# Kernel tuning notes

Measured on AMD Instinct MI355X. Metric: run time of the kernel, lower is better.

Reference implementation:

```python
import jax, jax.numpy as jnp
import numpy as np

B, S, E, H, D, P = 4, 2048, 1024, 16, 64, 64  # batch, seq, embed, heads, head_dim, position_dim
MASKED_BIAS = -10000.0


def setup_inputs() -> dict:
    key = jax.random.key(0)
    ks = jax.random.split(key, 24)
    n = lambda k, sh: jax.random.normal(k, sh, dtype=jnp.float32)
    eyeD = jnp.eye(D, dtype=jnp.float32)
    eyeH = jnp.eye(H, dtype=jnp.float32)
    inp = {
        'hidden_states': n(ks[0], (B, S, E)),
        'position_states': n(ks[1], (B, S, P)),
        # Conv2D per-head projections (identity init + perturbation): [H, D, D]
        'Wq': eyeD[None] + 0.02 * n(ks[2], (H, D, D)), 'bq': 0.01 * n(ks[3], (H, D)),
        'Wk': eyeD[None] + 0.02 * n(ks[4], (H, D, D)), 'bk': 0.01 * n(ks[5], (H, D)),
        'Wv': eyeD[None] + 0.02 * n(ks[6], (H, D, D)), 'bv': 0.01 * n(ks[7], (H, D)),
        # Conv2D(transpose=True) cross-head mix: weight [H_out, H_in, D], bias [H, D]
        'Wqh': eyeH[:, :, None] + 0.02 * n(ks[8], (H, H, D)), 'bqh': 0.01 * n(ks[9], (H, D)),
        'Wkh': eyeH[:, :, None] + 0.02 * n(ks[10], (H, H, D)), 'bkh': 0.01 * n(ks[11], (H, D)),
        'Wvh': eyeH[:, :, None] + 0.02 * n(ks[12], (H, H, D)), 'bvh': 0.01 * n(ks[13], (H, D)),
        # p_attn Conv1D: position_dim -> 3*head_dim
        'Wp': 0.02 * n(ks[14], (P, 3 * D)), 'bp': 0.01 * n(ks[15], (3 * D,)),
        # position_conv expand: weight [3, 1, H], bias [H]
        'Wpe': 0.02 * n(ks[16], (3, 1, H)), 'bpe': 0.01 * n(ks[17], (H,)),
        # c_proj Conv1D: E -> E
        'Wc': 0.02 * n(ks[18], (E, E)), 'bc': 0.01 * n(ks[19], (E,)),
    }
    return inp


def _attention(hidden_states, position_states, Wq, bq, Wqh, bqh, Wk, bk, Wkh, bkh,
               Wv, bv, Wvh, bvh, Wp, bp, Wpe, bpe, Wc, bc):
    b, s, _ = hidden_states.shape
    x = hidden_states.reshape(b, s, H, D)

    def proj(Wa, ba, Wh, bh):
        # Conv2D: per-head linear within head_dim
        y = jnp.einsum('bshd,hde->bshe', x, Wa) + ba
        # Conv2D(transpose): mix across heads, per feature dim d
        return jnp.einsum('bshd,ghd->bsgd', y, Wh) + bh

    q = proj(Wq, bq, Wqh, bqh)  # [b,s,H,D]
    k = proj(Wk, bk, Wkh, bkh)
    v = proj(Wv, bv, Wvh, bvh)

    # p_attn (Conv1D) -> [b,s,3,D]; p_expand broadcasts each var across heads
    p = (position_states @ Wp + bp).reshape(b, s, 3, D)
    pe = p[..., None, :] * Wpe[:, 0, :][:, :, None] + bpe[:, None]  # [b,s,3,H,D]
    q = q + pe[:, :, 0]
    k = k + pe[:, :, 1]
    v = v + pe[:, :, 2]

    q = q.transpose(0, 2, 1, 3)  # [b,H,s,D]
    k = k.transpose(0, 2, 1, 3)
    v = v.transpose(0, 2, 1, 3)

    scores = jnp.einsum('bhqd,bhkd->bhqk', q, k) / jnp.sqrt(jnp.float32(D))
    causal = jnp.tril(jnp.ones((s, s), dtype=bool))
    scores = jnp.where(causal, scores, jnp.float32(MASKED_BIAS))
    w = jax.nn.softmax(scores, axis=-1)
    o = jnp.einsum('bhqk,bhkd->bhqd', w, v)
    o = o.transpose(0, 2, 1, 3).reshape(b, s, E)
    return o @ Wc + bc


def reference(hidden_states, position_states, Wq, bq, Wqh, bqh, Wk, bk, Wkh, bkh,
              Wv, bv, Wvh, bvh, Wp, bp, Wpe, bpe, Wc, bc):
    return _attention(hidden_states, position_states, Wq, bq, Wqh, bqh, Wk, bk,
                      Wkh, bkh, Wv, bv, Wvh, bvh, Wp, bp, Wpe, bpe, Wc, bc)
```

## Files before the change

kernel.cpp:

```cpp
#include <hip/hip_runtime.h>
#include <stdint.h>
#include <stddef.h>

using bf16x8 = __attribute__((ext_vector_type(8))) __bf16;
using f32x4  = __attribute__((ext_vector_type(4))) float;
using u16x8  = __attribute__((ext_vector_type(8))) unsigned short;
using u16x4  = __attribute__((ext_vector_type(4))) unsigned short;
typedef unsigned short u16;

#define DEV __device__ __forceinline__

#define QSCALE 0.18033688011112042f
#define SBIAS 32.0f

DEV u16 f2bf(float f) {
  unsigned u = __float_as_uint(f);
  u += 0x7fffu + ((u >> 16) & 1u);
  return (u16)(u >> 16);
}

DEV void gld_lds16(const u16* g, u16* l) {
  __builtin_amdgcn_global_load_lds(
      (__attribute__((address_space(1))) void*)g,
      (__attribute__((address_space(3))) void*)l, 16, 0, 0);
}

__global__ __launch_bounds__(256) void k_packA(const float* __restrict__ hs,
                                               const float* __restrict__ ps,
                                               u16* __restrict__ A) {
  int idx = blockIdx.x * 256 + threadIdx.x;
  int t  = idx / 272;
  int c4 = (idx - t * 272) * 4;
  float4 f;
  if (c4 < 1024) f = *(const float4*)(hs + (size_t)t * 1024 + c4);
  else           f = *(const float4*)(ps + (size_t)t * 64 + (c4 - 1024));
  u16x4 o4;
  o4[0] = f2bf(f.x); o4[1] = f2bf(f.y); o4[2] = f2bf(f.z); o4[3] = f2bf(f.w);
  *(u16x4*)(A + (size_t)t * 1088 + c4) = o4;
}

__global__ __launch_bounds__(256) void k_buildW(const float* __restrict__ Wq, const float* __restrict__ Wk,
                                                const float* __restrict__ Wv, const float* __restrict__ Wqh,
                                                const float* __restrict__ Wkh, const float* __restrict__ Wvh,
                                                const float* __restrict__ Wp, const float* __restrict__ Wpe,
                                                u16* __restrict__ Wt) {
  int idx = blockIdx.x * 256 + threadIdx.x;
  int n = idx / 1088, kk = idx - n * 1088;
  int which = n >> 10, g = (n >> 6) & 15, e = n & 63;
  const float* Wa = (which == 0) ? Wq : (which == 1) ? Wk : Wv;
  const float* Wh = (which == 0) ? Wqh : (which == 1) ? Wkh : Wvh;
  float val;
  if (kk < 1024) {
    int h = kk >> 6, d = kk & 63;
    val = Wa[(size_t)(h * 64 + d) * 64 + e] * Wh[(size_t)(g * 16 + h) * 64 + e];
  } else {
    int p = kk - 1024;
    val = Wp[(size_t)p * 192 + which * 64 + e] * Wpe[which * 16 + g];
  }
  if (which == 0) val *= QSCALE;
  Wt[idx] = f2bf(val);
}

__global__ __launch_bounds__(256) void k_buildBias(const float* __restrict__ bq, const float* __restrict__ bk,
                                                   const float* __restrict__ bv, const float* __restrict__ Wqh,
                                                   const float* __restrict__ Wkh, const float* __restrict__ Wvh,
                                                   const float* __restrict__ bqh, const float* __restrict__ bkh,
                                                   const float* __restrict__ bvh, const float* __restrict__ bp,
                                                   const float* __restrict__ Wpe, const float* __restrict__ bpe,
                                                   float* __restrict__ bias) {
  int n = blockIdx.x * 256 + threadIdx.x;
  int which = n >> 10, g = (n >> 6) & 15, e = n & 63;
  const float* ba = (which == 0) ? bq : (which == 1) ? bk : bv;
  const float* Wh = (which == 0) ? Wqh : (which == 1) ? Wkh : Wvh;
  const float* bh = (which == 0) ? bqh : (which == 1) ? bkh : bvh;
  float s = bh[g * 64 + e] + bp[which * 64 + e] * Wpe[which * 16 + g] + bpe[g];
  for (int h = 0; h < 16; ++h) s += ba[h * 64 + e] * Wh[(g * 16 + h) * 64 + e];
  if (which == 0) s *= QSCALE;
  bias[n] = s;
}

__global__ __launch_bounds__(256) void k_transWc(const float* __restrict__ Wc, u16* __restrict__ WcT) {
  __shared__ float tile[32][33];
  int tx = threadIdx.x & 31, ty = threadIdx.x >> 5;
  int n0 = blockIdx.x * 32, k0 = blockIdx.y * 32;
#pragma unroll
  for (int i = 0; i < 32; i += 8)
    tile[ty + i][tx] = Wc[(size_t)(k0 + ty + i) * 1024 + n0 + tx];
  __syncthreads();
#pragma unroll
  for (int i = 0; i < 32; i += 8)
    WcT[(size_t)(n0 + ty + i) * 1024 + k0 + tx] = f2bf(tile[tx][ty + i]);
}

template <int EPI>
__global__ __launch_bounds__(256) void gemm128(const u16* __restrict__ A, const u16* __restrict__ Bt,
                                               const float* __restrict__ bias,
                                               u16* __restrict__ qo, u16* __restrict__ ko, u16* __restrict__ vo,
                                               float* __restrict__ outf, int M, int N, int K) {
  __shared__ alignas(16) u16 As[128 * 64];
  __shared__ alignas(16) u16 Bs[128 * 64];
  const int tid = threadIdx.x;
  const int l = tid & 63, w = tid >> 6;
  const int lr = l & 15, lg = l >> 4;
  const int wm = w >> 1, wn = w & 1;
  const int m0 = blockIdx.y * 128, n0 = blockIdx.x * 128;

  f32x4 acc[4][4] = {};
  const int KT = K >> 6;
  for (int kt = 0; kt < KT; ++kt) {
#pragma unroll
    for (int call = 0; call < 4; ++call) {
      int ci = (call * 4 + w) * 64 + l;
      int row = ci >> 3, s = ci & 7;
      int kq = (s ^ (row & 7)) * 8;
      gld_lds16(A + (size_t)(m0 + row) * K + kt * 64 + kq, &As[(call * 4 + w) * 512]);
      gld_lds16(Bt + (size_t)(n0 + row) * K + kt * 64 + kq, &Bs[(call * 4 + w) * 512]);
    }
    __syncthreads();
#pragma unroll
    for (int kk = 0; kk < 2; ++kk) {
      bf16x8 af[4], bfr[4];
#pragma unroll
      for (int mf = 0; mf < 4; ++mf) {
        int row = wm * 64 + mf * 16 + lr;
        int byo = row * 128 + (((kk * 32 + lg * 8) * 2) ^ ((row & 7) << 4));
        af[mf] = *(const bf16x8*)((const char*)As + byo);
      }
#pragma unroll
      for (int nf = 0; nf < 4; ++nf) {
        int row = wn * 64 + nf * 16 + lr;
        int byo = row * 128 + (((kk * 32 + lg * 8) * 2) ^ ((row & 7) << 4));
        bfr[nf] = *(const bf16x8*)((const char*)Bs + byo);
      }
#pragma unroll
      for (int mf = 0; mf < 4; ++mf)
#pragma unroll
        for (int nf = 0; nf < 4; ++nf)
          acc[mf][nf] = __builtin_amdgcn_mfma_f32_16x16x32_bf16(af[mf], bfr[nf], acc[mf][nf], 0, 0, 0);
    }
    __syncthreads();
  }
#pragma unroll
  for (int mf = 0; mf < 4; ++mf)
#pragma unroll
    for (int nf = 0; nf < 4; ++nf)
#pragma unroll
      for (int r = 0; r < 4; ++r) {
        int row = m0 + wm * 64 + mf * 16 + lg * 4 + r;
        int col = n0 + wn * 64 + nf * 16 + lr;
        float val = acc[mf][nf][r] + bias[col];
        if (EPI == 0) {
          int which = col >> 10, g = (col >> 6) & 15, e = col & 63;
          int b = row >> 11, si = row & 2047;
          size_t idx = ((size_t)((b * 16 + g) * 2048 + si)) * 64 + e;
          u16 bvv = f2bf(val);
          if (which == 0) qo[idx] = bvv;
          else if (which == 1) ko[idx] = bvv;
          else vo[idx] = bvv;
        } else {
          outf[(size_t)row * N + col] = val;
        }
      }
}

__global__ __launch_bounds__(256) void k_transV(const u16* __restrict__ v, u16* __restrict__ vT) {
  __shared__ u16 t[64][65];
  int bh = blockIdx.y, s0 = blockIdx.x * 64;
  const u16* src = v + ((size_t)bh * 2048 + s0) * 64;
  u16* dst = vT + (size_t)bh * 64 * 2048 + s0;
  int tid = threadIdx.x;
#pragma unroll
  for (int it = 0; it < 2; ++it) {
    int ci = it * 256 + tid;
    int row = ci >> 3, sl = ci & 7;
    u16x8 val = *(const u16x8*)(src + (size_t)row * 64 + sl * 8);
#pragma unroll
    for (int jj = 0; jj < 8; ++jj) t[row][sl * 8 + jj] = val[jj];
  }
  __syncthreads();
#pragma unroll
  for (int it = 0; it < 2; ++it) {
    int ci = it * 256 + tid;
    int d = ci >> 3, sl = ci & 7;
    u16x8 val;
#pragma unroll
    for (int jj = 0; jj < 8; ++jj) {
      int cp = sl * 8 + jj;
      int tt = (cp & 3) * 16 + (cp >> 2);
      val[jj] = t[tt][d];
    }
    *(u16x8*)(dst + (size_t)d * 2048 + sl * 8) = val;
  }
}

__global__ __launch_bounds__(512) void k_attn(const u16* __restrict__ q, const u16* __restrict__ k,
                                              const u16* __restrict__ vt, u16* __restrict__ o) {
  __shared__ alignas(16) u16 Ks[2][4096];
  __shared__ alignas(16) u16 Vs[2][4096];
  __shared__ alignas(16) u16 Ps[8][16 * 72];

  const int tid = threadIdx.x, l = tid & 63, w = tid >> 6;
  const int lr = l & 15, lg = l >> 4;
  const int i = blockIdx.x;
  const int bh = (i & 7) * 8 + ((i >> 3) & 7);
  const int xb = i >> 6;
  const int b = bh >> 4, h = bh & 15;

  const u16* qp = q + (size_t)bh * 2048 * 64;
  const u16* kp = k + (size_t)bh * 2048 * 64;
  const u16* vp = vt + (size_t)bh * 64 * 2048;

  const int srow = tid >> 3;
  const int skq = ((tid & 7) ^ (srow & 7)) * 8;

  bf16x8 ones;
#pragma unroll
  for (int e = 0; e < 8; ++e) ones[e] = (__bf16)1.0f;

  for (int half = 0; half < 2; ++half) {
    const int tile = half ? (15 - xb) : xb;
    const int qr0 = tile * 128 + w * 16;
    const int jmax = 2 * tile + 1;
    const int jmask = qr0 >> 6;

    bf16x8 qf[2];
#pragma unroll
    for (int kk = 0; kk < 2; ++kk)
      qf[kk] = *(const bf16x8*)(qp + (size_t)(qr0 + lr) * 64 + kk * 32 + lg * 8);

    f32x4 oacc[4] = {};
    f32x4 osum = {};

    gld_lds16(kp + (size_t)srow * 64 + skq, &Ks[0][w * 512]);
    gld_lds16(vp + (size_t)srow * 2048 + skq, &Vs[0][w * 512]);

    int cur = 0;
    for (int j = 0; j <= jmax; ++j) {
      if (j < jmax) {
        const int jn = j + 1;
        gld_lds16(kp + (size_t)(jn * 64 + srow) * 64 + skq, &Ks[cur ^ 1][w * 512]);
        gld_lds16(vp + (size_t)srow * 2048 + jn * 64 + skq, &Vs[cur ^ 1][w * 512]);
        asm volatile("s_waitcnt vmcnt(2)" ::: "memory");
      } else {
        asm volatile("s_waitcnt vmcnt(0)" ::: "memory");
      }
      __builtin_amdgcn_s_barrier();
      asm volatile("" ::: "memory");

      if (j <= jmask) {
        const u16* KsC = Ks[cur];
        const u16* VsC = Vs[cur];

        f32x4 sfr[4];
#pragma unroll
        for (int nf = 0; nf < 4; ++nf)
          sfr[nf] = f32x4{-SBIAS, -SBIAS, -SBIAS, -SBIAS};
#pragma unroll
        for (int kk = 0; kk < 2; ++kk) {
          bf16x8 bk[4];
#pragma unroll
          for (int nf = 0; nf < 4; ++nf) {
            int row = nf * 16 + lr;
            int byo = row * 128 + (((kk * 32 + lg * 8) * 2) ^ ((row & 7) << 4));
            bk[nf] = *(const bf16x8*)((const char*)KsC + byo);
          }
          __builtin_amdgcn_s_setprio(1);
#pragma unroll
          for (int nf = 0; nf < 4; ++nf)
            sfr[nf] = __builtin_amdgcn_mfma_f32_16x16x32_bf16(qf[kk], bk[nf], sfr[nf], 0, 0, 0);
          __builtin_amdgcn_s_setprio(0);
        }

        const bool maskt = (j == jmask);
#pragma unroll
        for (int r = 0; r < 4; ++r) {
          float s0 = sfr[0][r], s1 = sfr[1][r], s2 = sfr[2][r], s3 = sfr[3][r];
          if (maskt) {
            int rowg = qr0 + lg * 4 + r;
            int base = j * 64 + lr;
            if (base      > rowg) s0 = -1e30f;
            if (base + 16 > rowg) s1 = -1e30f;
            if (base + 32 > rowg) s2 = -1e30f;
            if (base + 48 > rowg) s3 = -1e30f;
          }
          float p0 = __builtin_amdgcn_exp2f(s0);
          float p1 = __builtin_amdgcn_exp2f(s1);
          float p2 = __builtin_amdgcn_exp2f(s2);
          float p3 = __builtin_amdgcn_exp2f(s3);
          unsigned w0, w1;
          asm("v_cvt_pk_bf16_f32 %0, %1, %2" : "=v"(w0) : "v"(p0), "v"(p1));
          asm("v_cvt_pk_bf16_f32 %0, %1, %2" : "=v"(w1) : "v"(p2), "v"(p3));
          uint2 pw; pw.x = w0; pw.y = w1;
          *(uint2*)&Ps[w][(lg * 4 + r) * 72 + 4 * lr] = pw;
        }

#pragma unroll
        for (int kk = 0; kk < 2; ++kk) {
          bf16x8 pa = *(const bf16x8*)&Ps[w][lr * 72 + kk * 32 + lg * 8];
          bf16x8 bv[4];
#pragma unroll
          for (int df = 0; df < 4; ++df) {
            int row = df * 16 + lr;
            int byo = row * 128 + (((kk * 32 + lg * 8) * 2) ^ ((row & 7) << 4));
            bv[df] = *(const bf16x8*)((const char*)VsC + byo);
          }
          __builtin_amdgcn_s_setprio(1);
#pragma unroll
          for (int df = 0; df < 4; ++df)
            oacc[df] = __builtin_amdgcn_mfma_f32_16x16x32_bf16(pa, bv[df], oacc[df], 0, 0, 0);
          osum = __builtin_amdgcn_mfma_f32_16x16x32_bf16(pa, ones, osum, 0, 0, 0);
          __builtin_amdgcn_s_setprio(0);
        }
      }

      asm volatile("s_waitcnt lgkmcnt(0)" ::: "memory");
      __builtin_amdgcn_s_barrier();
      asm volatile("" ::: "memory");
      cur ^= 1;
    }

#pragma unroll
    for (int r = 0; r < 4; ++r) {
      float inv = 1.0f / osum[r];
      int rowg = qr0 + lg * 4 + r;
#pragma unroll
      for (int df = 0; df < 4; ++df)
        o[((size_t)(b * 2048 + rowg)) * 1024 + h * 64 + df * 16 + lr] = f2bf(oacc[df][r] * inv);
    }
  }
}

extern "C" void kernel_launch(void* const* d_in, const int* in_sizes, int n_in,
                              void* d_out, int out_size, void* d_ws, size_t ws_size,
                              hipStream_t stream) {
  const float* hs  = (const float*)d_in[0];
  const float* pos = (const float*)d_in[1];
  const float* Wq  = (const float*)d_in[2];  const float* bq  = (const float*)d_in[3];
  const float* Wk  = (const float*)d_in[4];  const float* bk  = (const float*)d_in[5];
  const float* Wv  = (const float*)d_in[6];  const float* bv  = (const float*)d_in[7];
  const float* Wqh = (const float*)d_in[8];  const float* bqh = (const float*)d_in[9];
  const float* Wkh = (const float*)d_in[10]; const float* bkh = (const float*)d_in[11];
  const float* Wvh = (const float*)d_in[12]; const float* bvh = (const float*)d_in[13];
  const float* Wp  = (const float*)d_in[14]; const float* bp  = (const float*)d_in[15];
  const float* Wpe = (const float*)d_in[16]; const float* bpe = (const float*)d_in[17];
  const float* Wc  = (const float*)d_in[18]; const float* bc  = (const float*)d_in[19];
  float* out = (float*)d_out;
  char* ws = (char*)d_ws;

  u16*   Abf   = (u16*)  (ws + 0);
  u16*   WT    = (u16*)  (ws + 17825792);
  float* biasq = (float*)(ws + 24510464);
  u16*   WcT   = (u16*)  (ws + 24522752);
  u16*   qb_   = (u16*)  (ws + 26619904);
  u16*   kb_   = (u16*)  (ws + 43397120);
  u16*   vb_   = (u16*)  (ws + 60174336);
  u16*   vTb   = (u16*)  (ws + 76951552);
  u16*   ob    = Abf;

  k_packA<<<8704, 256, 0, stream>>>(hs, pos, Abf);
  k_buildW<<<13056, 256, 0, stream>>>(Wq, Wk, Wv, Wqh, Wkh, Wvh, Wp, Wpe, WT);
  k_buildBias<<<12, 256, 0, stream>>>(bq, bk, bv, Wqh, Wkh, Wvh, bqh, bkh, bvh, bp, Wpe, bpe, biasq);
  k_transWc<<<dim3(32, 32), 256, 0, stream>>>(Wc, WcT);
  gemm128<0><<<dim3(24, 64), 256, 0, stream>>>(Abf, WT, biasq, qb_, kb_, vb_, nullptr, 8192, 3072, 1088);
  k_transV<<<dim3(32, 64), 256, 0, stream>>>(vb_, vTb);
  k_attn<<<512, 512, 0, stream>>>(qb_, kb_, vTb, ob);
  gemm128<1><<<dim3(8, 64), 256, 0, stream>>>(ob, WcT, bc, nullptr, nullptr, nullptr, out, 8192, 1024, 1024);
}
```

Baseline: 186.9 us.

## Double-buffer GEMM LDS tiles and remap blocks across XCDs

The GEMM now keeps two LDS stages and prefetches the next K tile with global_load_lds while computing on the current one. Explicit vmcnt/lgkmcnt waits and raw barriers replace __syncthreads, and s_setprio raises priority around the MFMA block. Blocks move to a 1D grid with an XCD-aware remap so adjacent tiles land on the same chiplet's L2. The cost is double the LDS per block, which may lower occupancy, and more fragile hand-written synchronization.

```diff
diff --git a/kernel.cpp b/kernel.cpp
--- a/kernel.cpp
+++ b/kernel.cpp
@@ -96,27 +96,53 @@
 __global__ __launch_bounds__(256) void gemm128(const u16* __restrict__ A, const u16* __restrict__ Bt,
                                                const float* __restrict__ bias,
                                                u16* __restrict__ qo, u16* __restrict__ ko, u16* __restrict__ vo,
-                                               float* __restrict__ outf, int M, int N, int K) {
-  __shared__ alignas(16) u16 As[128 * 64];
-  __shared__ alignas(16) u16 Bs[128 * 64];
+                                               float* __restrict__ outf, int M, int N, int K, int NT) {
+  __shared__ alignas(16) u16 As[2][8192];
+  __shared__ alignas(16) u16 Bs[2][8192];
   const int tid = threadIdx.x;
   const int l = tid & 63, w = tid >> 6;
   const int lr = l & 15, lg = l >> 4;
   const int wm = w >> 1, wn = w & 1;
-  const int m0 = blockIdx.y * 128, n0 = blockIdx.x * 128;
+
+  const int nwg = gridDim.x;
+  const int cpx = nwg >> 3;
+  const int virt = (blockIdx.x & 7) * cpx + (blockIdx.x >> 3);
+  const int m0 = (virt / NT) * 128, n0 = (virt - (virt / NT) * NT) * 128;
+
+  const int KT = K >> 6;
 
   f32x4 acc[4][4] = {};
-  const int KT = K >> 6;
+
+#pragma unroll
+  for (int call = 0; call < 4; ++call) {
+    int ci = (call * 4 + w) * 64 + l;
+    int row = ci >> 3, s = ci & 7;
+    int kq = (s ^ (row & 7)) * 8;
+    gld_lds16(A + (size_t)(m0 + row) * K + kq, &As[0][(call * 4 + w) * 512]);
+    gld_lds16(Bt + (size_t)(n0 + row) * K + kq, &Bs[0][(call * 4 + w) * 512]);
+  }
+
+  int cur = 0;
   for (int kt = 0; kt < KT; ++kt) {
-#pragma unroll
-    for (int call = 0; call < 4; ++call) {
-      int ci = (call * 4 + w) * 64 + l;
-      int row = ci >> 3, s = ci & 7;
-      int kq = (s ^ (row & 7)) * 8;
-      gld_lds16(A + (size_t)(m0 + row) * K + kt * 64 + kq, &As[(call * 4 + w) * 512]);
-      gld_lds16(Bt + (size_t)(n0 + row) * K + kt * 64 + kq, &Bs[(call * 4 + w) * 512]);
+    if (kt + 1 < KT) {
+      const int kb = (kt + 1) * 64;
+#pragma unroll
+      for (int call = 0; call < 4; ++call) {
+        int ci = (call * 4 + w) * 64 + l;
+        int row = ci >> 3, s = ci & 7;
+        int kq = (s ^ (row & 7)) * 8;
+        gld_lds16(A + (size_t)(m0 + row) * K + kb + kq, &As[cur ^ 1][(call * 4 + w) * 512]);
+        gld_lds16(Bt + (size_t)(n0 + row) * K + kb + kq, &Bs[cur ^ 1][(call * 4 + w) * 512]);
+      }
+      asm volatile("s_waitcnt vmcnt(8)" ::: "memory");
+    } else {
+      asm volatile("s_waitcnt vmcnt(0)" ::: "memory");
     }
-    __syncthreads();
+    __builtin_amdgcn_s_barrier();
+    asm volatile("" ::: "memory");
+
+    const u16* AsC = As[cur];
+    const u16* BsC = Bs[cur];
 #pragma unroll
     for (int kk = 0; kk < 2; ++kk) {
       bf16x8 af[4], bfr[4];
@@ -124,22 +150,29 @@
       for (int mf = 0; mf < 4; ++mf) {
         int row = wm * 64 + mf * 16 + lr;
         int byo = row * 128 + (((kk * 32 + lg * 8) * 2) ^ ((row & 7) << 4));
-        af[mf] = *(const bf16x8*)((const char*)As + byo);
+        af[mf] = *(const bf16x8*)((const char*)AsC + byo);
       }
 #pragma unroll
       for (int nf = 0; nf < 4; ++nf) {
         int row = wn * 64 + nf * 16 + lr;
         int byo = row * 128 + (((kk * 32 + lg * 8) * 2) ^ ((row & 7) << 4));
-        bfr[nf] = *(const bf16x8*)((const char*)Bs + byo);
-      }
+        bfr[nf] = *(const bf16x8*)((const char*)BsC + byo);
+      }
+      __builtin_amdgcn_s_setprio(1);
 #pragma unroll
       for (int mf = 0; mf < 4; ++mf)
 #pragma unroll
         for (int nf = 0; nf < 4; ++nf)
           acc[mf][nf] = __builtin_amdgcn_mfma_f32_16x16x32_bf16(af[mf], bfr[nf], acc[mf][nf], 0, 0, 0);
+      __builtin_amdgcn_s_setprio(0);
     }
-    __syncthreads();
-  }
+
+    asm volatile("s_waitcnt lgkmcnt(0)" ::: "memory");
+    __builtin_amdgcn_s_barrier();
+    asm volatile("" ::: "memory");
+    cur ^= 1;
+  }
+
 #pragma unroll
   for (int mf = 0; mf < 4; ++mf)
 #pragma unroll
@@ -361,8 +394,8 @@
   k_buildW<<<13056, 256, 0, stream>>>(Wq, Wk, Wv, Wqh, Wkh, Wvh, Wp, Wpe, WT);
   k_buildBias<<<12, 256, 0, stream>>>(bq, bk, bv, Wqh, Wkh, Wvh, bqh, bkh, bvh, bp, Wpe, bpe, biasq);
   k_transWc<<<dim3(32, 32), 256, 0, stream>>>(Wc, WcT);
-  gemm128<0><<<dim3(24, 64), 256, 0, stream>>>(Abf, WT, biasq, qb_, kb_, vb_, nullptr, 8192, 3072, 1088);
+  gemm128<0><<<1536, 256, 0, stream>>>(Abf, WT, biasq, qb_, kb_, vb_, nullptr, 8192, 3072, 1088, 24);
   k_transV<<<dim3(32, 64), 256, 0, stream>>>(vb_, vTb);
   k_attn<<<512, 512, 0, stream>>>(qb_, kb_, vTb, ob);
-  gemm128<1><<<dim3(8, 64), 256, 0, stream>>>(ob, WcT, bc, nullptr, nullptr, nullptr, out, 8192, 1024, 1024);
-}
+  gemm128<1><<<512, 256, 0, stream>>>(ob, WcT, bc, nullptr, nullptr, nullptr, out, 8192, 1024, 1024, 8);
+}
```

Measured after the change: 179.4 us. 4.0% less time.
